# Optimization experiments

Hardware: AMD Instinct MI355X
Metric: run time of the kernel (lower is better)

Reference implementation:

```python
import jax, jax.numpy as jnp
import numpy as np

B, N, V, H, Z = 2048, 32, 10, 256, 64


def setup_inputs() -> dict:
    key = jax.random.key(0)
    ks = jax.random.split(key, 14)
    # strictly upper-triangular random DAG adjacency (topological order = vertex index)
    p = jax.random.uniform(ks[0], (B, N, N))
    tri = jnp.triu(jnp.ones((N, N), jnp.float32), k=1)
    adj = (p < 0.12).astype(jnp.float32) * tri
    node_types = jax.random.randint(ks[1], (B, N), 0, V).astype(jnp.int32)
    s = 0.05
    return dict(
        adj=adj,
        node_types=node_types,
        w_ih=jax.random.normal(ks[2], (V, 3 * H), jnp.float32) * s,
        w_hh=jax.random.normal(ks[3], (H, 3 * H), jnp.float32) * s,
        b_ih=jax.random.normal(ks[4], (3 * H,), jnp.float32) * s,
        b_hh=jax.random.normal(ks[5], (3 * H,), jnp.float32) * s,
        w_gate=jax.random.normal(ks[6], (H, H), jnp.float32) * s,
        b_gate=jax.random.normal(ks[7], (H,), jnp.float32) * s,
        w_map=jax.random.normal(ks[8], (H, H), jnp.float32) * s,
        w_mu=jax.random.normal(ks[9], (H, Z), jnp.float32) * s,
        b_mu=jax.random.normal(ks[10], (Z,), jnp.float32) * s,
        w_std=jax.random.normal(ks[11], (H, Z), jnp.float32) * s,
        b_std=jax.random.normal(ks[12], (Z,), jnp.float32) * s,
    )


def _gru_cell(x, h, w_ih, w_hh, b_ih, b_hh):
    # torch GRUCell math; weights stored [in, 3H]
    gi = x @ w_ih + b_ih  # [B, 3H]
    gh = h @ w_hh + b_hh
    i_r, i_z, i_n = jnp.split(gi, 3, axis=-1)
    h_r, h_z, h_n = jnp.split(gh, 3, axis=-1)
    r = jax.nn.sigmoid(i_r + h_r)
    z = jax.nn.sigmoid(i_z + h_z)
    n = jnp.tanh(i_n + r * h_n)
    return (1.0 - z) * n + z * h


def reference(adj, node_types, w_ih, w_hh, b_ih, b_hh, w_gate, b_gate, w_map,
              w_mu, b_mu, w_std, b_std):
    x_all = jax.nn.one_hot(node_types, V, dtype=adj.dtype)  # [B, N, V]
    hidden0 = jnp.zeros((B, N, H), adj.dtype)
    adj_cols = jnp.transpose(adj, (2, 0, 1))  # [N, B, N]; col v = predecessor mask of v
    x_seq = jnp.transpose(x_all, (1, 0, 2))   # [N, B, V]

    def step(hidden, inps):
        col, x, v = inps
        # gate(h_pred) * map(h_pred), summed over predecessors. map has no bias,
        # so non-predecessor (zero-masked) rows contribute exactly zero, matching
        # the padded-gather formulation in the original code.
        gm = jax.nn.sigmoid(hidden @ w_gate + b_gate) * (hidden @ w_map)  # [B, N, H]
        agg = jnp.einsum('bn,bnh->bh', col, gm)  # [B, H]; zero for v=0 (no preds)
        h_new = _gru_cell(x, agg, w_ih, w_hh, b_ih, b_hh)  # [B, H]
        hidden = jax.lax.dynamic_update_slice(hidden, h_new[:, None, :], (0, v, 0))
        return hidden, None

    hidden, _ = jax.lax.scan(step, hidden0, (adj_cols, x_seq, jnp.arange(N)))
    hg = hidden[:, -1, :]  # graph state = last vertex hidden
    mu = hg @ w_mu + b_mu
    sigma = hg @ w_std + b_std
    return (mu, sigma)
```

## Files before the change

kernel.cpp:

```cpp
#include <hip/hip_runtime.h>


#define BB 2048
#define NN 32
#define VV 10
#define HH 256
#define ZZ 64
#define BT 8
#define KC 8
#define NT1 48
#define NT2 32
#define WHH_ELEMS (NT1 * KC * 64 * 8)
#define WGM_ELEMS (NT2 * KC * 64 * 8)

typedef __attribute__((ext_vector_type(8))) short frag8;
typedef __attribute__((ext_vector_type(4))) float facc4;
typedef __attribute__((ext_vector_type(4))) unsigned short us4;
typedef __attribute__((ext_vector_type(4))) unsigned int ui4;

__device__ __forceinline__ float bf2f(unsigned short u) {
    unsigned int x = ((unsigned int)u) << 16;
    return __builtin_bit_cast(float, x);
}
__device__ __forceinline__ unsigned short f2bf(float f) {
    unsigned int x = __builtin_bit_cast(unsigned int, f);
    x += 0x7FFFu + ((x >> 16) & 1u);
    return (unsigned short)(x >> 16);
}
__device__ __forceinline__ float sigm(float x) { return 1.0f / (1.0f + __expf(-x)); }
__device__ __forceinline__ float ldv(const float* p, size_t i) { return p[i]; }
__device__ __forceinline__ float ldv(const unsigned short* p, size_t i) { return bf2f(p[i]); }
__device__ __forceinline__ void stv(float* p, size_t i, float v) { p[i] = v; }
__device__ __forceinline__ void stv(unsigned short* p, size_t i, float v) { p[i] = f2bf(v); }

__device__ __forceinline__ void pin_frag(frag8& f) {
    ui4 t = __builtin_bit_cast(ui4, f);
    asm volatile("" : "+v"(t));
    f = __builtin_bit_cast(frag8, t);
}

__global__ void detect_dtype(const unsigned short* __restrict__ w, int* flag) {
    __shared__ int zc, bc;
    if (threadIdx.x == 0) { zc = 0; bc = 0; }
    __syncthreads();
    int z = 0, b = 0;
    for (int i = threadIdx.x; i < 2048; i += 256) {
        unsigned short lo = w[2 * i];
        if (lo == 0) z++;
        unsigned e = (lo >> 7) & 0xFFu;
        if (e >= 0x86u) b++;
    }
    atomicAdd(&zc, z); atomicAdd(&bc, b);
    __syncthreads();
    if (threadIdx.x == 0) *flag = (bc > 0 || zc > 512) ? 1 : 0;
}

template <typename T>
__global__ void repack_weights(const T* __restrict__ w_hh,
                               const T* __restrict__ w_gate,
                               const T* __restrict__ w_map,
                               const T* __restrict__ w_ih,
                               const T* __restrict__ b_ih,
                               unsigned short* __restrict__ whh_p,
                               unsigned short* __restrict__ wgm_p,
                               float* __restrict__ wihG,
                               const int* __restrict__ flag, int want) {
    if (*flag != want) return;
    int t = blockIdx.x * blockDim.x + threadIdx.x;
    int lane = t & 63;
    int frag = t >> 6;
    int kbase = (lane >> 4) * 8;
    if (frag < NT1 * KC) {
        int jt = frag / KC, kc = frag % KC;
        int col = jt * 16 + (lane & 15);
        unsigned short* dst = whh_p + ((size_t)frag * 64 + lane) * 8;
        #pragma unroll
        for (int j = 0; j < 8; ++j)
            dst[j] = f2bf(ldv(w_hh, (size_t)(kc * 32 + kbase + j) * 768 + col));
    } else if (frag < (NT1 + NT2) * KC) {
        int f2 = frag - NT1 * KC;
        int jt = f2 / KC, kc = f2 % KC;
        int col = jt * 16 + (lane & 15);
        unsigned short* dst = wgm_p + ((size_t)f2 * 64 + lane) * 8;
        #pragma unroll
        for (int j = 0; j < 8; ++j) {
            int k = kc * 32 + kbase + j;
            dst[j] = f2bf((col < HH) ? ldv(w_gate, (size_t)k * HH + col)
                                     : ldv(w_map, (size_t)k * HH + (col - HH)));
        }
    } else {
        int idx = t - (NT1 + NT2) * KC * 64;
        if (idx < VV * 768) {
            int c = idx % 768;
            wihG[idx] = ldv(w_ih, (size_t)idx) + ldv(b_ih, (size_t)c);
        }
    }
}

template <typename T>
__global__ __launch_bounds__(1024, 4) void vae_main(
    const T* __restrict__ adj,
    const int* __restrict__ ntypes,
    const T* __restrict__ b_hh,
    const T* __restrict__ b_gate,
    const T* __restrict__ w_mu,
    const T* __restrict__ b_mu,
    const T* __restrict__ w_std,
    const T* __restrict__ b_std,
    const unsigned short* __restrict__ whh_p,
    const unsigned short* __restrict__ wgm_p,
    const float* __restrict__ wihG,
    T* __restrict__ out,
    const int* __restrict__ flag, int want)
{
    if (*flag != want) return;

    __shared__ __align__(16) unsigned short gmAll[BT][NN][HH];
    __shared__ __align__(16) unsigned short aggbf[16][264];
    __shared__ __align__(16) unsigned short hnew[16][264];
    __shared__ unsigned int  amask[BT][NN];
    __shared__ int           ntva[BT][NN];
    __shared__ __align__(16) float bhhL[768];
    __shared__ float bgL[HH];

    float* const aggA = (float*)&aggbf[8][0];
    float* const aggB = (float*)&hnew[8][0];

    const int tid  = threadIdx.x;
    const int lane = tid & 63;
    const int w    = tid >> 6;
    const int b0   = blockIdx.x * BT;

    const frag8* whh8 = (const frag8*)whh_p;
    const frag8* wgm8 = (const frag8*)wgm_p;

    if (tid < 256) {
        int bi = tid >> 5, vv = tid & 31;
        unsigned m = 0;
        for (int n = 0; n < NN; ++n)
            if (ldv(adj, ((size_t)(b0 + bi) * NN + n) * NN + vv) != 0.0f) m |= (1u << n);
        amask[bi][vv] = m;
    } else if (tid < 512) {
        int idx = tid - 256;
        int bi = idx >> 5, vv = idx & 31;
        ntva[bi][vv] = ntypes[(b0 + bi) * NN + vv];
    }
    for (int i = tid; i < 768; i += 1024) bhhL[i] = ldv(b_hh, i);
    if (tid < HH) bgL[tid] = ldv(b_gate, tid);

    frag8 wG[KC], wM[KC];
    {
        const frag8* pG = wgm8 + (size_t)(w     ) * (KC * 64) + lane;
        const frag8* pM = wgm8 + (size_t)(w + 16) * (KC * 64) + lane;
        #pragma unroll
        for (int kc = 0; kc < KC; ++kc) { wG[kc] = pG[kc * 64]; wM[kc] = pM[kc * 64]; }
        #pragma unroll
        for (int kc = 0; kc < KC; ++kc) { pin_frag(wG[kc]); pin_frag(wM[kc]); }
    }
    __syncthreads();

    for (int v = 0; v < NN; ++v) {
        if (w < BT) {
            const int bi = w;
            const int h4 = lane * 4;
            unsigned m = amask[bi][v];
            float a0 = 0.f, a1 = 0.f, a2 = 0.f, a3 = 0.f;
            const unsigned short* rb = &gmAll[bi][0][0] + h4;
            while (m) {
                const int n0 = __builtin_ctz(m); m &= m - 1;
                const us4 g0 = *(const us4*)(rb + n0 * HH);
                if (m) {
                    const int n1 = __builtin_ctz(m); m &= m - 1;
                    const us4 g1 = *(const us4*)(rb + n1 * HH);
                    a0 += bf2f(g0.x) + bf2f(g1.x);
                    a1 += bf2f(g0.y) + bf2f(g1.y);
                    a2 += bf2f(g0.z) + bf2f(g1.z);
                    a3 += bf2f(g0.w) + bf2f(g1.w);
                } else {
                    a0 += bf2f(g0.x); a1 += bf2f(g0.y);
                    a2 += bf2f(g0.z); a3 += bf2f(g0.w);
                }
            }
            float* ap = (bi < 4) ? (aggA + bi * 256) : (aggB + (bi - 4) * 256);
            *(float4*)(ap + h4) = make_float4(a0, a1, a2, a3);
            ushort4 ab; ab.x = f2bf(a0); ab.y = f2bf(a1); ab.z = f2bf(a2); ab.w = f2bf(a3);
            *(ushort4*)&aggbf[bi][h4] = ab;
        }
        __syncthreads();

        {
            const int t = w;
            const int col = t * 16 + (lane & 15);
            const int q = lane >> 4;

            facc4 aR = {0.f, 0.f, 0.f, 0.f};
            facc4 aZ = {0.f, 0.f, 0.f, 0.f};
            facc4 aN = {0.f, 0.f, 0.f, 0.f};
            const frag8* pR = whh8 + (size_t)(t     ) * (KC * 64) + lane;
            const frag8* pZ = whh8 + (size_t)(t + 16) * (KC * 64) + lane;
            const frag8* pN = whh8 + (size_t)(t + 32) * (KC * 64) + lane;
            #pragma unroll
            for (int kc = 0; kc < KC; ++kc) {
                const frag8 af = *(const frag8*)&aggbf[lane & 15][kc * 32 + (lane >> 4) * 8];
                aR = __builtin_amdgcn_mfma_f32_16x16x32_bf16(af, pR[kc * 64], aR, 0, 0, 0);
                aZ = __builtin_amdgcn_mfma_f32_16x16x32_bf16(af, pZ[kc * 64], aZ, 0, 0, 0);
                aN = __builtin_amdgcn_mfma_f32_16x16x32_bf16(af, pN[kc * 64], aN, 0, 0, 0);
            }
            if (q < 2) {
                const float bhr = bhhL[col], bhz = bhhL[col + 256], bhn = bhhL[col + 512];
                const float* ap = (q == 0) ? aggA : aggB;
                #pragma unroll
                for (int i = 0; i < 4; ++i) {
                    const float* wr = wihG + (size_t)ntva[4 * q + i][v] * 768 + col;
                    const float r = sigm(wr[0]   + aR[i] + bhr);
                    const float z = sigm(wr[256] + aZ[i] + bhz);
                    const float n = tanhf(wr[512] + r * (aN[i] + bhn));
                    hnew[4 * q + i][col] = f2bf((1.f - z) * n + z * ap[i * 256 + col]);
                }
            }
        }
        __syncthreads();

        {
            facc4 aG = {0.f, 0.f, 0.f, 0.f};
            facc4 aM = {0.f, 0.f, 0.f, 0.f};
            #pragma unroll
            for (int kc = 0; kc < KC; ++kc) {
                const frag8 hf = *(const frag8*)&hnew[lane & 15][kc * 32 + (lane >> 4) * 8];
                aG = __builtin_amdgcn_mfma_f32_16x16x32_bf16(hf, wG[kc], aG, 0, 0, 0);
                aM = __builtin_amdgcn_mfma_f32_16x16x32_bf16(hf, wM[kc], aM, 0, 0, 0);
            }
            const int col = w * 16 + (lane & 15);
            const int q = lane >> 4;
            if (q < 2) {
                const float bg = bgL[col];
                #pragma unroll
                for (int i = 0; i < 4; ++i)
                    gmAll[4 * q + i][v][col] = f2bf(sigm(aG[i] + bg) * aM[i]);
            }
        }
        __syncthreads();
    }

    {
        const int bi = w >> 1, half = w & 1, z = lane;
        float am = 0.f, as = 0.f;
        const int h0 = half * 128;
        #pragma unroll 4
        for (int h = h0; h < h0 + 128; ++h) {
            const float hv = bf2f(hnew[bi][h]);
            am += hv * ldv(w_mu, (size_t)h * ZZ + z);
            as += hv * ldv(w_std, (size_t)h * ZZ + z);
        }
        float* sc = (bi < 4) ? (aggA + bi * 256) : (aggB + (bi - 4) * 256);
        sc[half * 64 + z]       = am;
        sc[128 + half * 64 + z] = as;
    }
    __syncthreads();
    if (w < BT) {
        const int bi = w, z = lane;
        const float* sc = (bi < 4) ? (aggA + bi * 256) : (aggB + (bi - 4) * 256);
        const float am = sc[z] + sc[64 + z] + ldv(b_mu, z);
        const float as = sc[128 + z] + sc[192 + z] + ldv(b_std, z);
        stv(out, (size_t)(b0 + bi) * ZZ + z, am);
        stv(out, (size_t)BB * ZZ + (size_t)(b0 + bi) * ZZ + z, as);
    }
}

extern "C" void kernel_launch(void* const* d_in, const int* in_sizes, int n_in,
                              void* d_out, int out_size, void* d_ws, size_t ws_size,
                              hipStream_t stream)
{
    unsigned short* whh_p = (unsigned short*)d_ws;
    unsigned short* wgm_p = whh_p + WHH_ELEMS;
    float* wihG = (float*)(wgm_p + WGM_ELEMS);

    size_t flag_off = (ws_size >= 8) ? ((ws_size - 4) & ~(size_t)3) : 0;
    int* flag = (int*)((char*)d_ws + flag_off);

    detect_dtype<<<dim3(1), 256, 0, stream>>>((const unsigned short*)d_in[2], flag);

    repack_weights<float><<<dim3(190), 256, 0, stream>>>(
        (const float*)d_in[3], (const float*)d_in[6], (const float*)d_in[8],
        (const float*)d_in[2], (const float*)d_in[4],
        whh_p, wgm_p, wihG, flag, 1);
    repack_weights<unsigned short><<<dim3(190), 256, 0, stream>>>(
        (const unsigned short*)d_in[3], (const unsigned short*)d_in[6],
        (const unsigned short*)d_in[8], (const unsigned short*)d_in[2],
        (const unsigned short*)d_in[4],
        whh_p, wgm_p, wihG, flag, 0);

    vae_main<float><<<dim3(BB / BT), 1024, 0, stream>>>(
        (const float*)d_in[0], (const int*)d_in[1],
        (const float*)d_in[5], (const float*)d_in[7],
        (const float*)d_in[9], (const float*)d_in[10],
        (const float*)d_in[11], (const float*)d_in[12],
        whh_p, wgm_p, wihG, (float*)d_out, flag, 1);
    vae_main<unsigned short><<<dim3(BB / BT), 1024, 0, stream>>>(
        (const unsigned short*)d_in[0], (const int*)d_in[1],
        (const unsigned short*)d_in[5], (const unsigned short*)d_in[7],
        (const unsigned short*)d_in[9], (const unsigned short*)d_in[10],
        (const unsigned short*)d_in[11], (const unsigned short*)d_in[12],
        whh_p, wgm_p, wihG, (unsigned short*)d_out, flag, 0);
}
```

Measured before the change: 529.1 us.

## Halve block to 512 threads and pin W_hh fragments in registers instead of W_gate/W_map

Shrinks each block from 16 to 8 waves, so each wave now computes two column tiles for both the GRU and gate/map matmuls. The larger W_hh slice (6x8 frags per wave) is kept resident in registers, and the gate/map weights are streamed from global/L2 each step. The mu/sigma head is done by one wave per batch row without the split reduction. This trades register pressure (waves_per_eu 2) and fewer waves to hide latency for no per-step W_hh reloads, with gate/map weights now reloaded each step.

Measured after the change: 601.8 us. 13.7% more time.

```diff
diff --git a/kernel.cpp b/kernel.cpp
--- a/kernel.cpp
+++ b/kernel.cpp
@@ -98,7 +98,9 @@
 }
 
 template <typename T>
-__global__ __launch_bounds__(1024, 4) void vae_main(
+__global__ __launch_bounds__(512)
+__attribute__((amdgpu_waves_per_eu(2, 2)))
+void vae_main(
     const T* __restrict__ adj,
     const int* __restrict__ ntypes,
     const T* __restrict__ b_hh,
@@ -140,27 +142,31 @@
         for (int n = 0; n < NN; ++n)
             if (ldv(adj, ((size_t)(b0 + bi) * NN + n) * NN + vv) != 0.0f) m |= (1u << n);
         amask[bi][vv] = m;
-    } else if (tid < 512) {
+    } else {
         int idx = tid - 256;
         int bi = idx >> 5, vv = idx & 31;
         ntva[bi][vv] = ntypes[(b0 + bi) * NN + vv];
     }
-    for (int i = tid; i < 768; i += 1024) bhhL[i] = ldv(b_hh, i);
+    for (int i = tid; i < 768; i += 512) bhhL[i] = ldv(b_hh, i);
     if (tid < HH) bgL[tid] = ldv(b_gate, tid);
 
-    frag8 wG[KC], wM[KC];
-    {
-        const frag8* pG = wgm8 + (size_t)(w     ) * (KC * 64) + lane;
-        const frag8* pM = wgm8 + (size_t)(w + 16) * (KC * 64) + lane;
-        #pragma unroll
-        for (int kc = 0; kc < KC; ++kc) { wG[kc] = pG[kc * 64]; wM[kc] = pM[kc * 64]; }
-        #pragma unroll
-        for (int kc = 0; kc < KC; ++kc) { pin_frag(wG[kc]); pin_frag(wM[kc]); }
-    }
+    frag8 wHH[6][KC];
+    #pragma unroll
+    for (int s = 0; s < 2; ++s)
+        #pragma unroll
+        for (int g = 0; g < 3; ++g) {
+            const frag8* p = whh8 + (size_t)(w + 8 * s + 16 * g) * (KC * 64) + lane;
+            #pragma unroll
+            for (int kc = 0; kc < KC; ++kc) wHH[s * 3 + g][kc] = p[kc * 64];
+        }
+    #pragma unroll
+    for (int i = 0; i < 6; ++i)
+        #pragma unroll
+        for (int kc = 0; kc < KC; ++kc) pin_frag(wHH[i][kc]);
     __syncthreads();
 
     for (int v = 0; v < NN; ++v) {
-        if (w < BT) {
+        {
             const int bi = w;
             const int h4 = lane * 4;
             unsigned m = amask[bi][v];
@@ -188,23 +194,21 @@
         }
         __syncthreads();
 
-        {
-            const int t = w;
+        #pragma unroll
+        for (int s = 0; s < 2; ++s) {
+            const int t = w + 8 * s;
             const int col = t * 16 + (lane & 15);
             const int q = lane >> 4;
 
             facc4 aR = {0.f, 0.f, 0.f, 0.f};
             facc4 aZ = {0.f, 0.f, 0.f, 0.f};
             facc4 aN = {0.f, 0.f, 0.f, 0.f};
-            const frag8* pR = whh8 + (size_t)(t     ) * (KC * 64) + lane;
-            const frag8* pZ = whh8 + (size_t)(t + 16) * (KC * 64) + lane;
-            const frag8* pN = whh8 + (size_t)(t + 32) * (KC * 64) + lane;
             #pragma unroll
             for (int kc = 0; kc < KC; ++kc) {
                 const frag8 af = *(const frag8*)&aggbf[lane & 15][kc * 32 + (lane >> 4) * 8];
-                aR = __builtin_amdgcn_mfma_f32_16x16x32_bf16(af, pR[kc * 64], aR, 0, 0, 0);
-                aZ = __builtin_amdgcn_mfma_f32_16x16x32_bf16(af, pZ[kc * 64], aZ, 0, 0, 0);
-                aN = __builtin_amdgcn_mfma_f32_16x16x32_bf16(af, pN[kc * 64], aN, 0, 0, 0);
+                aR = __builtin_amdgcn_mfma_f32_16x16x32_bf16(af, wHH[s * 3 + 0][kc], aR, 0, 0, 0);
+                aZ = __builtin_amdgcn_mfma_f32_16x16x32_bf16(af, wHH[s * 3 + 1][kc], aZ, 0, 0, 0);
+                aN = __builtin_amdgcn_mfma_f32_16x16x32_bf16(af, wHH[s * 3 + 2][kc], aN, 0, 0, 0);
             }
             if (q < 2) {
                 const float bhr = bhhL[col], bhz = bhhL[col + 256], bhn = bhhL[col + 512];
@@ -222,48 +226,48 @@
         __syncthreads();
 
         {
-            facc4 aG = {0.f, 0.f, 0.f, 0.f};
-            facc4 aM = {0.f, 0.f, 0.f, 0.f};
+            facc4 aG0 = {0.f, 0.f, 0.f, 0.f};
+            facc4 aG1 = {0.f, 0.f, 0.f, 0.f};
+            facc4 aM0 = {0.f, 0.f, 0.f, 0.f};
+            facc4 aM1 = {0.f, 0.f, 0.f, 0.f};
+            const frag8* pG0 = wgm8 + (size_t)(w     ) * (KC * 64) + lane;
+            const frag8* pG1 = wgm8 + (size_t)(w +  8) * (KC * 64) + lane;
+            const frag8* pM0 = wgm8 + (size_t)(w + 16) * (KC * 64) + lane;
+            const frag8* pM1 = wgm8 + (size_t)(w + 24) * (KC * 64) + lane;
             #pragma unroll
             for (int kc = 0; kc < KC; ++kc) {
                 const frag8 hf = *(const frag8*)&hnew[lane & 15][kc * 32 + (lane >> 4) * 8];
-                aG = __builtin_amdgcn_mfma_f32_16x16x32_bf16(hf, wG[kc], aG, 0, 0, 0);
-                aM = __builtin_amdgcn_mfma_f32_16x16x32_bf16(hf, wM[kc], aM, 0, 0, 0);
-            }
-            const int col = w * 16 + (lane & 15);
+                aG0 = __builtin_amdgcn_mfma_f32_16x16x32_bf16(hf, pG0[kc * 64], aG0, 0, 0, 0);
+                aG1 = __builtin_amdgcn_mfma_f32_16x16x32_bf16(hf, pG1[kc * 64], aG1, 0, 0, 0);
+                aM0 = __builtin_amdgcn_mfma_f32_16x16x32_bf16(hf, pM0[kc * 64], aM0, 0, 0, 0);
+                aM1 = __builtin_amdgcn_mfma_f32_16x16x32_bf16(hf, pM1[kc * 64], aM1, 0, 0, 0);
+            }
             const int q = lane >> 4;
             if (q < 2) {
-                const float bg = bgL[col];
+                const int c0 = w * 16 + (lane & 15);
+                const int c1 = (w + 8) * 16 + (lane & 15);
+                const float bg0 = bgL[c0], bg1 = bgL[c1];
                 #pragma unroll
-                for (int i = 0; i < 4; ++i)
-                    gmAll[4 * q + i][v][col] = f2bf(sigm(aG[i] + bg) * aM[i]);
+                for (int i = 0; i < 4; ++i) {
+                    gmAll[4 * q + i][v][c0] = f2bf(sigm(aG0[i] + bg0) * aM0[i]);
+                    gmAll[4 * q + i][v][c1] = f2bf(sigm(aG1[i] + bg1) * aM1[i]);
+                }
             }
         }
         __syncthreads();
     }
 
     {
-        const int bi = w >> 1, half = w & 1, z = lane;
+        const int bi = w, z = lane;
         float am = 0.f, as = 0.f;
-        const int h0 = half * 128;
         #pragma unroll 4
-        for (int h = h0; h < h0 + 128; ++h) {
+        for (int h = 0; h < HH; ++h) {
             const float hv = bf2f(hnew[bi][h]);
             am += hv * ldv(w_mu, (size_t)h * ZZ + z);
             as += hv * ldv(w_std, (size_t)h * ZZ + z);
         }
-        float* sc = (bi < 4) ? (aggA + bi * 256) : (aggB + (bi - 4) * 256);
-        sc[half * 64 + z]       = am;
-        sc[128 + half * 64 + z] = as;
-    }
-    __syncthreads();
-    if (w < BT) {
-        const int bi = w, z = lane;
-        const float* sc = (bi < 4) ? (aggA + bi * 256) : (aggB + (bi - 4) * 256);
-        const float am = sc[z] + sc[64 + z] + ldv(b_mu, z);
-        const float as = sc[128 + z] + sc[192 + z] + ldv(b_std, z);
-        stv(out, (size_t)(b0 + bi) * ZZ + z, am);
-        stv(out, (size_t)BB * ZZ + (size_t)(b0 + bi) * ZZ + z, as);
+        stv(out, (size_t)(b0 + bi) * ZZ + z, am + ldv(b_mu, z));
+        stv(out, (size_t)BB * ZZ + (size_t)(b0 + bi) * ZZ + z, as + ldv(b_std, z));
     }
 }
 
@@ -290,13 +294,13 @@
         (const unsigned short*)d_in[4],
         whh_p, wgm_p, wihG, flag, 0);
 
-    vae_main<float><<<dim3(BB / BT), 1024, 0, stream>>>(
+    vae_main<float><<<dim3(BB / BT), 512, 0, stream>>>(
         (const float*)d_in[0], (const int*)d_in[1],
         (const float*)d_in[5], (const float*)d_in[7],
         (const float*)d_in[9], (const float*)d_in[10],
         (const float*)d_in[11], (const float*)d_in[12],
         whh_p, wgm_p, wihG, (float*)d_out, flag, 1);
-    vae_main<unsigned short><<<dim3(BB / BT), 1024, 0, stream>>>(
+    vae_main<unsigned short><<<dim3(BB / BT), 512, 0, stream>>>(
         (const unsigned short*)d_in[0], (const int*)d_in[1],
         (const unsigned short*)d_in[5], (const unsigned short*)d_in[7],
         (const unsigned short*)d_in[9], (const unsigned short*)d_in[10],
```

## Precompute predecessor aggregation early and hoist GRU input-weight loads before MFMAs

Applied to the files above, without the earlier changes.

The predecessor sum for vertex v+1, covering every predecessor except v, is now accumulated at the end of step v, right after the gate/map stage. The aggregation phase then only adds the vertex v-1 contribution, which shortens that serialized phase between barriers. The one-hot w_ih row loads are moved ahead of the W_hh MFMA loop so their global latency overlaps the matrix work. Adjacency reads use nontemporal loads. The change adds register pressure from the carried partial sums and the prefetched inputs. It also reads gmAll rows written by other waves in the same phase, which may rely on barrier ordering.

Result: slower. 539.8 us (+2.0%).

```diff
diff --git a/kernel.cpp b/kernel.cpp
--- a/kernel.cpp
+++ b/kernel.cpp
@@ -30,6 +30,12 @@
 __device__ __forceinline__ float sigm(float x) { return 1.0f / (1.0f + __expf(-x)); }
 __device__ __forceinline__ float ldv(const float* p, size_t i) { return p[i]; }
 __device__ __forceinline__ float ldv(const unsigned short* p, size_t i) { return bf2f(p[i]); }
+__device__ __forceinline__ float ntldv(const float* p, size_t i) {
+    return __builtin_nontemporal_load(p + i);
+}
+__device__ __forceinline__ float ntldv(const unsigned short* p, size_t i) {
+    return bf2f(__builtin_nontemporal_load(p + i));
+}
 __device__ __forceinline__ void stv(float* p, size_t i, float v) { p[i] = v; }
 __device__ __forceinline__ void stv(unsigned short* p, size_t i, float v) { p[i] = f2bf(v); }
 
@@ -138,7 +144,7 @@
         int bi = tid >> 5, vv = tid & 31;
         unsigned m = 0;
         for (int n = 0; n < NN; ++n)
-            if (ldv(adj, ((size_t)(b0 + bi) * NN + n) * NN + vv) != 0.0f) m |= (1u << n);
+            if (ntldv(adj, ((size_t)(b0 + bi) * NN + n) * NN + vv) != 0.0f) m |= (1u << n);
         amask[bi][vv] = m;
     } else if (tid < 512) {
         int idx = tid - 256;
@@ -159,31 +165,21 @@
     }
     __syncthreads();
 
+    float pa0 = 0.f, pa1 = 0.f, pa2 = 0.f, pa3 = 0.f;
+    const int h4 = lane * 4;
+
     for (int v = 0; v < NN; ++v) {
         if (w < BT) {
             const int bi = w;
-            const int h4 = lane * 4;
-            unsigned m = amask[bi][v];
-            float a0 = 0.f, a1 = 0.f, a2 = 0.f, a3 = 0.f;
-            const unsigned short* rb = &gmAll[bi][0][0] + h4;
-            while (m) {
-                const int n0 = __builtin_ctz(m); m &= m - 1;
-                const us4 g0 = *(const us4*)(rb + n0 * HH);
-                if (m) {
-                    const int n1 = __builtin_ctz(m); m &= m - 1;
-                    const us4 g1 = *(const us4*)(rb + n1 * HH);
-                    a0 += bf2f(g0.x) + bf2f(g1.x);
-                    a1 += bf2f(g0.y) + bf2f(g1.y);
-                    a2 += bf2f(g0.z) + bf2f(g1.z);
-                    a3 += bf2f(g0.w) + bf2f(g1.w);
-                } else {
-                    a0 += bf2f(g0.x); a1 += bf2f(g0.y);
-                    a2 += bf2f(g0.z); a3 += bf2f(g0.w);
-                }
+            if (v > 0 && ((amask[bi][v] >> (v - 1)) & 1u)) {
+                const us4 g = *(const us4*)(&gmAll[bi][v - 1][0] + h4);
+                pa0 += bf2f(g.x); pa1 += bf2f(g.y);
+                pa2 += bf2f(g.z); pa3 += bf2f(g.w);
             }
             float* ap = (bi < 4) ? (aggA + bi * 256) : (aggB + (bi - 4) * 256);
-            *(float4*)(ap + h4) = make_float4(a0, a1, a2, a3);
-            ushort4 ab; ab.x = f2bf(a0); ab.y = f2bf(a1); ab.z = f2bf(a2); ab.w = f2bf(a3);
+            *(float4*)(ap + h4) = make_float4(pa0, pa1, pa2, pa3);
+            ushort4 ab; ab.x = f2bf(pa0); ab.y = f2bf(pa1);
+            ab.z = f2bf(pa2); ab.w = f2bf(pa3);
             *(ushort4*)&aggbf[bi][h4] = ab;
         }
         __syncthreads();
@@ -192,6 +188,15 @@
             const int t = w;
             const int col = t * 16 + (lane & 15);
             const int q = lane >> 4;
+
+            float xr[4], xz[4], xn[4];
+            if (q < 2) {
+                #pragma unroll
+                for (int i = 0; i < 4; ++i) {
+                    const float* wr = wihG + (size_t)ntva[4 * q + i][v] * 768 + col;
+                    xr[i] = wr[0]; xz[i] = wr[256]; xn[i] = wr[512];
+                }
+            }
 
             facc4 aR = {0.f, 0.f, 0.f, 0.f};
             facc4 aZ = {0.f, 0.f, 0.f, 0.f};
@@ -211,10 +216,9 @@
                 const float* ap = (q == 0) ? aggA : aggB;
                 #pragma unroll
                 for (int i = 0; i < 4; ++i) {
-                    const float* wr = wihG + (size_t)ntva[4 * q + i][v] * 768 + col;
-                    const float r = sigm(wr[0]   + aR[i] + bhr);
-                    const float z = sigm(wr[256] + aZ[i] + bhz);
-                    const float n = tanhf(wr[512] + r * (aN[i] + bhn));
+                    const float r = sigm(xr[i] + aR[i] + bhr);
+                    const float z = sigm(xz[i] + aZ[i] + bhz);
+                    const float n = tanhf(xn[i] + r * (aN[i] + bhn));
                     hnew[4 * q + i][col] = f2bf((1.f - z) * n + z * ap[i * 256 + col]);
                 }
             }
@@ -237,6 +241,27 @@
                 #pragma unroll
                 for (int i = 0; i < 4; ++i)
                     gmAll[4 * q + i][v][col] = f2bf(sigm(aG[i] + bg) * aM[i]);
+            }
+
+            pa0 = pa1 = pa2 = pa3 = 0.f;
+            if (w < BT && v + 1 < NN) {
+                unsigned m = amask[w][v + 1] & ((v > 0) ? ((1u << v) - 1u) : 0u);
+                const unsigned short* rb = &gmAll[w][0][0] + h4;
+                while (m) {
+                    const int n0 = __builtin_ctz(m); m &= m - 1;
+                    const us4 g0 = *(const us4*)(rb + n0 * HH);
+                    if (m) {
+                        const int n1 = __builtin_ctz(m); m &= m - 1;
+                        const us4 g1 = *(const us4*)(rb + n1 * HH);
+                        pa0 += bf2f(g0.x) + bf2f(g1.x);
+                        pa1 += bf2f(g0.y) + bf2f(g1.y);
+                        pa2 += bf2f(g0.z) + bf2f(g1.z);
+                        pa3 += bf2f(g0.w) + bf2f(g1.w);
+                    } else {
+                        pa0 += bf2f(g0.x); pa1 += bf2f(g0.y);
+                        pa2 += bf2f(g0.z); pa3 += bf2f(g0.w);
+                    }
+                }
             }
         }
         __syncthreads();
```
